# Kernel tuning notes

Hardware: AMD Instinct MI355X
Metric: run time of the kernel (lower is better)

## Reference

```python
import jax, jax.numpy as jnp
import numpy as np

B, L = 131072, 24  # batch size, number of links (= n_dofs, all revolute)


def _skew(v):
    # v: [L, 3] -> [L, 3, 3] cross-product matrices
    zeros = jnp.zeros_like(v[:, 0])
    return jnp.stack([
        jnp.stack([zeros, -v[:, 2], v[:, 1]], axis=-1),
        jnp.stack([v[:, 2], zeros, -v[:, 0]], axis=-1),
        jnp.stack([-v[:, 1], v[:, 0], zeros], axis=-1),
    ], axis=-2)


def setup_inputs() -> dict:
    key = jax.random.key(0)
    k1, k2, k3, k4 = jax.random.split(key, 4)
    q = jax.random.normal(k1, (B, L), dtype=jnp.float32)
    qd = jax.random.normal(k2, (B, L), dtype=jnp.float32)
    axes = jax.random.normal(k3, (L, 3), dtype=jnp.float32)   # joint axes (normalized in reference)
    t_fix = jax.random.normal(k4, (L, 3), dtype=jnp.float32)  # fixed parent->joint translations
    return {"q": q, "qd": qd, "axes": axes, "t_fix": t_fix}


def reference(q, qd, axes, t_fix):
    # Stateless forward kinematics for all links of a serial revolute chain.
    # joint_pose_i = Trans(t_fix_i) @ Rot(axis_i, q_i);  pose_i = pose_{i-1} @ joint_pose_i
    dtype = q.dtype
    a = axes / jnp.linalg.norm(axes, axis=-1, keepdims=True)  # [L,3]
    K = _skew(a)                                              # [L,3,3]
    KK = jnp.einsum('lij,ljk->lik', K, K)
    s = jnp.sin(q)[..., None, None]                           # [B,L,1,1]
    c = jnp.cos(q)[..., None, None]
    I3 = jnp.eye(3, dtype=dtype)
    # Rodrigues: per-joint rotation [B,L,3,3]
    R_joint = I3 + s * K[None] + (1.0 - c) * KK[None]

    def step(carry, x):
        Rp, tp = carry          # parent pose: [B,3,3], [B,3]
        Rj, tf = x              # joint rotation [B,3,3], fixed translation [3]
        tc = tp + jnp.einsum('bij,j->bi', Rp, tf)
        Rc = jnp.einsum('bij,bjk->bik', Rp, Rj)
        return (Rc, tc), (Rc, tc)

    R0 = jnp.broadcast_to(I3, (q.shape[0], 3, 3))
    t0 = jnp.zeros((q.shape[0], 3), dtype=dtype)
    Rj_seq = jnp.moveaxis(R_joint, 1, 0)                      # [L,B,3,3]
    _, (Rs, ts) = jax.lax.scan(step, (R0, t0), (Rj_seq, t_fix))
    Rs = jnp.moveaxis(Rs, 0, 1)                               # [B,L,3,3]
    ts = jnp.moveaxis(ts, 0, 1)                               # [B,L,3]
    top = jnp.concatenate([Rs, ts[..., None]], axis=-1)       # [B,L,3,4]
    bottom = jnp.broadcast_to(jnp.array([0., 0., 0., 1.], dtype=dtype),
                              top.shape[:-2] + (1, 4))
    return jnp.concatenate([top, bottom], axis=-2)            # [B,L,4,4]
```

## Files before the change

kernel.cpp:

```cpp
#include <hip/hip_runtime.h>


typedef float v4 __attribute__((ext_vector_type(4)));

constexpr int L = 24;

__global__ __launch_bounds__(256, 4) void fk_kernel(
    const float* __restrict__ q,
    const float* __restrict__ axes,
    const float* __restrict__ tfix,
    float* __restrict__ out,
    int nb)
{
    __shared__ float s_lnk[L][12];

    if (threadIdx.x < L) {
        const int l = threadIdx.x;
        float ax = axes[l * 3 + 0], ay = axes[l * 3 + 1], az = axes[l * 3 + 2];
        float inv = rsqrtf(ax * ax + ay * ay + az * az);
        ax *= inv; ay *= inv; az *= inv;
        s_lnk[l][0] = ax;             s_lnk[l][1] = ay;             s_lnk[l][2] = az;
        s_lnk[l][3] = tfix[l * 3 + 0]; s_lnk[l][4] = tfix[l * 3 + 1]; s_lnk[l][5] = tfix[l * 3 + 2];
        s_lnk[l][6] = ax * ax;        s_lnk[l][7] = ay * ay;
        s_lnk[l][8] = az * az;        s_lnk[l][9] = ax * ay;
        s_lnk[l][10] = ax * az;       s_lnk[l][11] = ay * az;
    }
    __syncthreads();

    const int tid = blockIdx.x * 256 + threadIdx.x;
    const int b = tid >> 2;
    const int r = tid & 3;
    if (b >= nb) return;

    float qv[L];
    {
        const v4* q4 = (const v4*)(q + (size_t)b * L);
        #pragma unroll
        for (int i = 0; i < L / 4; ++i) {
            v4 v = q4[i];
            qv[4 * i + 0] = v.x;
            qv[4 * i + 1] = v.y;
            qv[4 * i + 2] = v.z;
            qv[4 * i + 3] = v.w;
        }
    }

    float Ra = (r == 0) ? 1.f : 0.f;
    float Rb = (r == 1) ? 1.f : 0.f;
    float Rc = (r == 2) ? 1.f : 0.f;
    float t  = (r == 3) ? 1.f : 0.f;

    v4* orow = (v4*)out + (size_t)b * (4 * L) + r;

    #pragma unroll
    for (int l = 0; l < L; ++l) {
        const float ax = s_lnk[l][0], ay = s_lnk[l][1], az = s_lnk[l][2];
        const float fx = s_lnk[l][3], fy = s_lnk[l][4], fz = s_lnk[l][5];
        const float xx = s_lnk[l][6], yy = s_lnk[l][7], zz = s_lnk[l][8];
        const float xy = s_lnk[l][9], xz = s_lnk[l][10], yz = s_lnk[l][11];

        float s, c;
        __sincosf(qv[l], &s, &c);
        const float omc = 1.0f - c;

        const float J00 = fmaf(omc, xx, c);
        const float J11 = fmaf(omc, yy, c);
        const float J22 = fmaf(omc, zz, c);
        const float oxy = omc * xy, oxz = omc * xz, oyz = omc * yz;
        const float sx = s * ax, sy = s * ay, sz = s * az;
        const float J01 = oxy - sz, J10 = oxy + sz;
        const float J02 = oxz + sy, J20 = oxz - sy;
        const float J12 = oyz - sx, J21 = oyz + sx;

        t = fmaf(Ra, fx, fmaf(Rb, fy, fmaf(Rc, fz, t)));

        const float na  = fmaf(Ra, J00, fmaf(Rb, J10, Rc * J20));
        const float nb_ = fmaf(Ra, J01, fmaf(Rb, J11, Rc * J21));
        const float nc  = fmaf(Ra, J02, fmaf(Rb, J12, Rc * J22));
        Ra = na; Rb = nb_; Rc = nc;

        orow[l * 4] = v4{Ra, Rb, Rc, t};
    }
}

extern "C" void kernel_launch(void* const* d_in, const int* in_sizes, int n_in,
                              void* d_out, int out_size, void* d_ws, size_t ws_size,
                              hipStream_t stream) {
    const float* q    = (const float*)d_in[0];
    const float* axes = (const float*)d_in[2];
    const float* tfix = (const float*)d_in[3];
    float* out = (float*)d_out;

    const int nb = in_sizes[0] / L;
    const long long nthreads = (long long)nb * 4;
    const int grid = (int)((nthreads + 255) / 256);
    fk_kernel<<<grid, 256, 0, stream>>>(q, axes, tfix, out, nb);
}
```

Before: 214.0 us.

## Compute full pose per thread instead of one row per thread

Switches from four threads per batch element (one output row each) to one thread per batch element that carries the full 3x3 rotation and translation. This removes the fourfold redundant q loads and sincos evaluations and vectorizes the shared-memory constant reads. In exchange each thread writes 64 contiguous bytes per link with large strides between threads, which loses store coalescing. There are also fewer threads available for latency hiding, and launch bounds are relaxed to allow more registers.

```diff
diff --git a/kernel.cpp b/kernel.cpp
--- a/kernel.cpp
+++ b/kernel.cpp
@@ -5,31 +5,30 @@
 
 constexpr int L = 24;
 
-__global__ __launch_bounds__(256, 4) void fk_kernel(
+__global__ __launch_bounds__(256, 2) void fk_kernel(
     const float* __restrict__ q,
     const float* __restrict__ axes,
     const float* __restrict__ tfix,
     float* __restrict__ out,
     int nb)
 {
-    __shared__ float s_lnk[L][12];
+    __shared__ __align__(16) float s_lnk[L][16];
 
     if (threadIdx.x < L) {
         const int l = threadIdx.x;
         float ax = axes[l * 3 + 0], ay = axes[l * 3 + 1], az = axes[l * 3 + 2];
         float inv = rsqrtf(ax * ax + ay * ay + az * az);
         ax *= inv; ay *= inv; az *= inv;
-        s_lnk[l][0] = ax;             s_lnk[l][1] = ay;             s_lnk[l][2] = az;
+        s_lnk[l][0] = ax;              s_lnk[l][1] = ay;              s_lnk[l][2] = az;
         s_lnk[l][3] = tfix[l * 3 + 0]; s_lnk[l][4] = tfix[l * 3 + 1]; s_lnk[l][5] = tfix[l * 3 + 2];
-        s_lnk[l][6] = ax * ax;        s_lnk[l][7] = ay * ay;
-        s_lnk[l][8] = az * az;        s_lnk[l][9] = ax * ay;
-        s_lnk[l][10] = ax * az;       s_lnk[l][11] = ay * az;
+        s_lnk[l][6] = ax * ax;         s_lnk[l][7] = ay * ay;
+        s_lnk[l][8] = az * az;         s_lnk[l][9] = ax * ay;
+        s_lnk[l][10] = ax * az;        s_lnk[l][11] = ay * az;
+        s_lnk[l][12] = 0.f; s_lnk[l][13] = 0.f; s_lnk[l][14] = 0.f; s_lnk[l][15] = 0.f;
     }
     __syncthreads();
 
-    const int tid = blockIdx.x * 256 + threadIdx.x;
-    const int b = tid >> 2;
-    const int r = tid & 3;
+    const int b = blockIdx.x * 256 + threadIdx.x;
     if (b >= nb) return;
 
     float qv[L];
@@ -45,19 +44,21 @@
         }
     }
 
-    float Ra = (r == 0) ? 1.f : 0.f;
-    float Rb = (r == 1) ? 1.f : 0.f;
-    float Rc = (r == 2) ? 1.f : 0.f;
-    float t  = (r == 3) ? 1.f : 0.f;
+    float R00 = 1.f, R01 = 0.f, R02 = 0.f;
+    float R10 = 0.f, R11 = 1.f, R12 = 0.f;
+    float R20 = 0.f, R21 = 0.f, R22 = 1.f;
+    float tx = 0.f, ty = 0.f, tz = 0.f;
 
-    v4* orow = (v4*)out + (size_t)b * (4 * L) + r;
+    v4* obase = (v4*)out + (size_t)b * (4 * L);
 
     #pragma unroll
     for (int l = 0; l < L; ++l) {
-        const float ax = s_lnk[l][0], ay = s_lnk[l][1], az = s_lnk[l][2];
-        const float fx = s_lnk[l][3], fy = s_lnk[l][4], fz = s_lnk[l][5];
-        const float xx = s_lnk[l][6], yy = s_lnk[l][7], zz = s_lnk[l][8];
-        const float xy = s_lnk[l][9], xz = s_lnk[l][10], yz = s_lnk[l][11];
+        const v4 c0 = *(const v4*)&s_lnk[l][0];
+        const v4 c1 = *(const v4*)&s_lnk[l][4];
+        const v4 c2 = *(const v4*)&s_lnk[l][8];
+        const float ax = c0.x, ay = c0.y, az = c0.z, fx = c0.w;
+        const float fy = c1.x, fz = c1.y, xx = c1.z, yy = c1.w;
+        const float zz = c2.x, xy = c2.y, xz = c2.z, yz = c2.w;
 
         float s, c;
         __sincosf(qv[l], &s, &c);
@@ -72,14 +73,27 @@
         const float J02 = oxz + sy, J20 = oxz - sy;
         const float J12 = oyz - sx, J21 = oyz + sx;
 
-        t = fmaf(Ra, fx, fmaf(Rb, fy, fmaf(Rc, fz, t)));
+        tx = fmaf(R00, fx, fmaf(R01, fy, fmaf(R02, fz, tx)));
+        ty = fmaf(R10, fx, fmaf(R11, fy, fmaf(R12, fz, ty)));
+        tz = fmaf(R20, fx, fmaf(R21, fy, fmaf(R22, fz, tz)));
 
-        const float na  = fmaf(Ra, J00, fmaf(Rb, J10, Rc * J20));
-        const float nb_ = fmaf(Ra, J01, fmaf(Rb, J11, Rc * J21));
-        const float nc  = fmaf(Ra, J02, fmaf(Rb, J12, Rc * J22));
-        Ra = na; Rb = nb_; Rc = nc;
+        const float n00 = fmaf(R00, J00, fmaf(R01, J10, R02 * J20));
+        const float n01 = fmaf(R00, J01, fmaf(R01, J11, R02 * J21));
+        const float n02 = fmaf(R00, J02, fmaf(R01, J12, R02 * J22));
+        const float n10 = fmaf(R10, J00, fmaf(R11, J10, R12 * J20));
+        const float n11 = fmaf(R10, J01, fmaf(R11, J11, R12 * J21));
+        const float n12 = fmaf(R10, J02, fmaf(R11, J12, R12 * J22));
+        const float n20 = fmaf(R20, J00, fmaf(R21, J10, R22 * J20));
+        const float n21 = fmaf(R20, J01, fmaf(R21, J11, R22 * J21));
+        const float n22 = fmaf(R20, J02, fmaf(R21, J12, R22 * J22));
+        R00 = n00; R01 = n01; R02 = n02;
+        R10 = n10; R11 = n11; R12 = n12;
+        R20 = n20; R21 = n21; R22 = n22;
 
-        orow[l * 4] = v4{Ra, Rb, Rc, t};
+        obase[l * 4 + 0] = v4{R00, R01, R02, tx};
+        obase[l * 4 + 1] = v4{R10, R11, R12, ty};
+        obase[l * 4 + 2] = v4{R20, R21, R22, tz};
+        obase[l * 4 + 3] = v4{0.f, 0.f, 0.f, 1.f};
     }
 }
 
@@ -92,7 +106,6 @@
     float* out = (float*)d_out;
 
     const int nb = in_sizes[0] / L;
-    const long long nthreads = (long long)nb * 4;
-    const int grid = (int)((nthreads + 255) / 256);
+    const int grid = (nb + 255) / 256;
     fk_kernel<<<grid, 256, 0, stream>>>(q, axes, tfix, out, nb);
 }
```

Result: slower. 251.6 us (+17.6%).

## Stage output poses through LDS per wave for coalesced nontemporal stores

Applied to the files above, without the earlier changes.

Each wave writes its computed 4x4 poses for 16 batch elements into a padded LDS buffer in chunks of 8 links. It then reads them back so consecutive lanes write contiguous 16-byte segments of global memory with nontemporal stores. The goal is to replace the previous strided per-thread row stores with fully coalesced writes. The q load is also moved ahead of the shared-memory setup barrier, and link constants are read as vector LDS loads. The cost is extra LDS traffic and footprint, and the wave-level sync relies only on a compiler memory barrier within the wave.

```diff
diff --git a/kernel.cpp b/kernel.cpp
--- a/kernel.cpp
+++ b/kernel.cpp
@@ -4,6 +4,11 @@
 typedef float v4 __attribute__((ext_vector_type(4)));
 
 constexpr int L = 24;
+constexpr int CHUNK = 8;
+constexpr int NCHUNK = L / CHUNK;
+constexpr int CW  = CHUNK * 16;
+constexpr int CWP = CW + 4;
+constexpr int WAVE_WORDS = 16 * CWP;
 
 __global__ __launch_bounds__(256, 4) void fk_kernel(
     const float* __restrict__ q,
@@ -12,74 +17,110 @@
     float* __restrict__ out,
     int nb)
 {
-    __shared__ float s_lnk[L][12];
+    __shared__ __align__(16) float s_lnk[L][16];
+    __shared__ __align__(16) float s_buf[4 * WAVE_WORDS];
 
-    if (threadIdx.x < L) {
-        const int l = threadIdx.x;
-        float ax = axes[l * 3 + 0], ay = axes[l * 3 + 1], az = axes[l * 3 + 2];
-        float inv = rsqrtf(ax * ax + ay * ay + az * az);
-        ax *= inv; ay *= inv; az *= inv;
-        s_lnk[l][0] = ax;             s_lnk[l][1] = ay;             s_lnk[l][2] = az;
-        s_lnk[l][3] = tfix[l * 3 + 0]; s_lnk[l][4] = tfix[l * 3 + 1]; s_lnk[l][5] = tfix[l * 3 + 2];
-        s_lnk[l][6] = ax * ax;        s_lnk[l][7] = ay * ay;
-        s_lnk[l][8] = az * az;        s_lnk[l][9] = ax * ay;
-        s_lnk[l][10] = ax * az;       s_lnk[l][11] = ay * az;
-    }
-    __syncthreads();
-
-    const int tid = blockIdx.x * 256 + threadIdx.x;
-    const int b = tid >> 2;
-    const int r = tid & 3;
-    if (b >= nb) return;
+    const int tid  = threadIdx.x;
+    const int wave = tid >> 6;
+    const int lane = tid & 63;
+    const int e    = lane >> 2;
+    const int r    = lane & 3;
+    const int wave_elem0 = blockIdx.x * 64 + wave * 16;
+    const int b = wave_elem0 + e;
 
     float qv[L];
-    {
+    if (b < nb) {
         const v4* q4 = (const v4*)(q + (size_t)b * L);
         #pragma unroll
         for (int i = 0; i < L / 4; ++i) {
             v4 v = q4[i];
-            qv[4 * i + 0] = v.x;
-            qv[4 * i + 1] = v.y;
-            qv[4 * i + 2] = v.z;
-            qv[4 * i + 3] = v.w;
+            qv[4*i+0] = v.x; qv[4*i+1] = v.y; qv[4*i+2] = v.z; qv[4*i+3] = v.w;
         }
     }
+
+    if (tid < L) {
+        const int l = tid;
+        float ax = axes[l*3+0], ay = axes[l*3+1], az = axes[l*3+2];
+        float inv = rsqrtf(ax*ax + ay*ay + az*az);
+        ax *= inv; ay *= inv; az *= inv;
+        s_lnk[l][0] = ax;            s_lnk[l][1] = ay;            s_lnk[l][2] = az;
+        s_lnk[l][3] = tfix[l*3+0];   s_lnk[l][4] = tfix[l*3+1];   s_lnk[l][5] = tfix[l*3+2];
+        s_lnk[l][6] = ax*ax;         s_lnk[l][7] = ay*ay;
+        s_lnk[l][8] = az*az;         s_lnk[l][9] = ax*ay;
+        s_lnk[l][10] = ax*az;        s_lnk[l][11] = ay*az;
+        s_lnk[l][12] = 0.f; s_lnk[l][13] = 0.f; s_lnk[l][14] = 0.f; s_lnk[l][15] = 0.f;
+    }
+    __syncthreads();
 
     float Ra = (r == 0) ? 1.f : 0.f;
     float Rb = (r == 1) ? 1.f : 0.f;
     float Rc = (r == 2) ? 1.f : 0.f;
     float t  = (r == 3) ? 1.f : 0.f;
 
-    v4* orow = (v4*)out + (size_t)b * (4 * L) + r;
+    float* wbuf = s_buf + wave * WAVE_WORDS;
+    v4* lrow = (v4*)(wbuf + e * CWP + r * 4);
 
     #pragma unroll
-    for (int l = 0; l < L; ++l) {
-        const float ax = s_lnk[l][0], ay = s_lnk[l][1], az = s_lnk[l][2];
-        const float fx = s_lnk[l][3], fy = s_lnk[l][4], fz = s_lnk[l][5];
-        const float xx = s_lnk[l][6], yy = s_lnk[l][7], zz = s_lnk[l][8];
-        const float xy = s_lnk[l][9], xz = s_lnk[l][10], yz = s_lnk[l][11];
+    for (int chunk = 0; chunk < NCHUNK; ++chunk) {
+        if (b < nb) {
+            #pragma unroll
+            for (int lc = 0; lc < CHUNK; ++lc) {
+                const int l = chunk * CHUNK + lc;
+                const v4 c0 = *(const v4*)&s_lnk[l][0];
+                const v4 c1 = *(const v4*)&s_lnk[l][4];
+                const v4 c2 = *(const v4*)&s_lnk[l][8];
+                const float ax = c0.x, ay = c0.y, az = c0.z, fx = c0.w;
+                const float fy = c1.x, fz = c1.y, xx = c1.z, yy = c1.w;
+                const float zz = c2.x, xy = c2.y, xz = c2.z, yz = c2.w;
 
-        float s, c;
-        __sincosf(qv[l], &s, &c);
-        const float omc = 1.0f - c;
+                float s, c;
+                __sincosf(qv[l], &s, &c);
+                const float omc = 1.0f - c;
 
-        const float J00 = fmaf(omc, xx, c);
-        const float J11 = fmaf(omc, yy, c);
-        const float J22 = fmaf(omc, zz, c);
-        const float oxy = omc * xy, oxz = omc * xz, oyz = omc * yz;
-        const float sx = s * ax, sy = s * ay, sz = s * az;
-        const float J01 = oxy - sz, J10 = oxy + sz;
-        const float J02 = oxz + sy, J20 = oxz - sy;
-        const float J12 = oyz - sx, J21 = oyz + sx;
+                const float J00 = fmaf(omc, xx, c);
+                const float J11 = fmaf(omc, yy, c);
+                const float J22 = fmaf(omc, zz, c);
+                const float oxy = omc * xy, oxz = omc * xz, oyz = omc * yz;
+                const float sx = s * ax, sy = s * ay, sz = s * az;
+                const float J01 = oxy - sz, J10 = oxy + sz;
+                const float J02 = oxz + sy, J20 = oxz - sy;
+                const float J12 = oyz - sx, J21 = oyz + sx;
 
-        t = fmaf(Ra, fx, fmaf(Rb, fy, fmaf(Rc, fz, t)));
+                t = fmaf(Ra, fx, fmaf(Rb, fy, fmaf(Rc, fz, t)));
 
-        const float na  = fmaf(Ra, J00, fmaf(Rb, J10, Rc * J20));
-        const float nb_ = fmaf(Ra, J01, fmaf(Rb, J11, Rc * J21));
-        const float nc  = fmaf(Ra, J02, fmaf(Rb, J12, Rc * J22));
-        Ra = na; Rb = nb_; Rc = nc;
+                const float na  = fmaf(Ra, J00, fmaf(Rb, J10, Rc * J20));
+                const float nb_ = fmaf(Ra, J01, fmaf(Rb, J11, Rc * J21));
+                const float nc  = fmaf(Ra, J02, fmaf(Rb, J12, Rc * J22));
+                Ra = na; Rb = nb_; Rc = nc;
 
-        orow[l * 4] = v4{Ra, Rb, Rc, t};
+                lrow[lc * 4] = v4{Ra, Rb, Rc, t};
+            }
+        }
+
+        asm volatile("" ::: "memory");
+
+        float* gbase = out + (size_t)wave_elem0 * 384 + chunk * CW;
+        if (wave_elem0 + 15 < nb) {
+            #pragma unroll
+            for (int j = 0; j < CHUNK; ++j) {
+                const unsigned w = j * 256 + lane * 4;
+                const unsigned elem = w >> 7;
+                const unsigned rem  = w & 127u;
+                v4 v = *(const v4*)(wbuf + elem * CWP + rem);
+                __builtin_nontemporal_store(v, (v4*)(gbase + (size_t)elem * 384 + rem));
+            }
+        } else if (wave_elem0 < nb) {
+            #pragma unroll
+            for (int j = 0; j < CHUNK; ++j) {
+                const unsigned w = j * 256 + lane * 4;
+                const unsigned elem = w >> 7;
+                const unsigned rem  = w & 127u;
+                if (wave_elem0 + (int)elem < nb) {
+                    v4 v = *(const v4*)(wbuf + elem * CWP + rem);
+                    __builtin_nontemporal_store(v, (v4*)(gbase + (size_t)elem * 384 + rem));
+                }
+            }
+        }
     }
 }
 
@@ -92,7 +133,6 @@
     float* out = (float*)d_out;
 
     const int nb = in_sizes[0] / L;
-    const long long nthreads = (long long)nb * 4;
-    const int grid = (int)((nthreads + 255) / 256);
+    const int grid = (nb + 63) / 64;
     fk_kernel<<<grid, 256, 0, stream>>>(q, axes, tfix, out, nb);
 }
```

Result: slower. 224.0 us (+4.7%).

## Use persistent grid-stride blocks with prefetch of next batch's joint angles

Applied to the files above, without the earlier changes.

Launches a fixed grid of 512 blocks that loop over batch elements with a grid stride instead of one thread group per element. Each iteration prefetches the next element's joint angles into registers so the global load overlaps the current chain computation. Per-link constants are padded to 16 floats so they can be read from shared memory as vector loads. The risk is fewer resident waves to hide the latency of the output stores, which dominate this bandwidth-bound kernel, plus extra register pressure from the prefetch buffers.

```diff
diff --git a/kernel.cpp b/kernel.cpp
--- a/kernel.cpp
+++ b/kernel.cpp
@@ -4,6 +4,8 @@
 typedef float v4 __attribute__((ext_vector_type(4)));
 
 constexpr int L = 24;
+constexpr int BLOCKS = 512;
+constexpr int NGROUPS = BLOCKS * 64;
 
 __global__ __launch_bounds__(256, 4) void fk_kernel(
     const float* __restrict__ q,
@@ -12,74 +14,97 @@
     float* __restrict__ out,
     int nb)
 {
-    __shared__ float s_lnk[L][12];
+    __shared__ __align__(16) float s_lnk[L][16];
 
     if (threadIdx.x < L) {
         const int l = threadIdx.x;
-        float ax = axes[l * 3 + 0], ay = axes[l * 3 + 1], az = axes[l * 3 + 2];
-        float inv = rsqrtf(ax * ax + ay * ay + az * az);
+        float ax = axes[l*3+0], ay = axes[l*3+1], az = axes[l*3+2];
+        float inv = rsqrtf(ax*ax + ay*ay + az*az);
         ax *= inv; ay *= inv; az *= inv;
-        s_lnk[l][0] = ax;             s_lnk[l][1] = ay;             s_lnk[l][2] = az;
-        s_lnk[l][3] = tfix[l * 3 + 0]; s_lnk[l][4] = tfix[l * 3 + 1]; s_lnk[l][5] = tfix[l * 3 + 2];
-        s_lnk[l][6] = ax * ax;        s_lnk[l][7] = ay * ay;
-        s_lnk[l][8] = az * az;        s_lnk[l][9] = ax * ay;
-        s_lnk[l][10] = ax * az;       s_lnk[l][11] = ay * az;
+        s_lnk[l][0] = ax;            s_lnk[l][1] = ay;            s_lnk[l][2] = az;
+        s_lnk[l][3] = tfix[l*3+0];   s_lnk[l][4] = tfix[l*3+1];   s_lnk[l][5] = tfix[l*3+2];
+        s_lnk[l][6] = ax*ax;         s_lnk[l][7] = ay*ay;
+        s_lnk[l][8] = az*az;         s_lnk[l][9] = ax*ay;
+        s_lnk[l][10] = ax*az;        s_lnk[l][11] = ay*az;
+        s_lnk[l][12] = 0.f; s_lnk[l][13] = 0.f; s_lnk[l][14] = 0.f; s_lnk[l][15] = 0.f;
     }
     __syncthreads();
 
     const int tid = blockIdx.x * 256 + threadIdx.x;
-    const int b = tid >> 2;
-    const int r = tid & 3;
+    const int gid = tid >> 2;
+    const int r   = tid & 3;
+
+    int b = gid;
     if (b >= nb) return;
 
-    float qv[L];
-    {
-        const v4* q4 = (const v4*)(q + (size_t)b * L);
+    const v4* q4 = (const v4*)q;
+
+    v4 nq0 = q4[(size_t)b * 6 + 0];
+    v4 nq1 = q4[(size_t)b * 6 + 1];
+    v4 nq2 = q4[(size_t)b * 6 + 2];
+    v4 nq3 = q4[(size_t)b * 6 + 3];
+    v4 nq4 = q4[(size_t)b * 6 + 4];
+    v4 nq5 = q4[(size_t)b * 6 + 5];
+
+    while (b < nb) {
+        float qv[L];
+        qv[0]=nq0.x; qv[1]=nq0.y; qv[2]=nq0.z; qv[3]=nq0.w;
+        qv[4]=nq1.x; qv[5]=nq1.y; qv[6]=nq1.z; qv[7]=nq1.w;
+        qv[8]=nq2.x; qv[9]=nq2.y; qv[10]=nq2.z; qv[11]=nq2.w;
+        qv[12]=nq3.x; qv[13]=nq3.y; qv[14]=nq3.z; qv[15]=nq3.w;
+        qv[16]=nq4.x; qv[17]=nq4.y; qv[18]=nq4.z; qv[19]=nq4.w;
+        qv[20]=nq5.x; qv[21]=nq5.y; qv[22]=nq5.z; qv[23]=nq5.w;
+
+        const int bn = b + NGROUPS;
+        if (bn < nb) {
+            nq0 = q4[(size_t)bn * 6 + 0];
+            nq1 = q4[(size_t)bn * 6 + 1];
+            nq2 = q4[(size_t)bn * 6 + 2];
+            nq3 = q4[(size_t)bn * 6 + 3];
+            nq4 = q4[(size_t)bn * 6 + 4];
+            nq5 = q4[(size_t)bn * 6 + 5];
+        }
+
+        float Ra = (r == 0) ? 1.f : 0.f;
+        float Rb = (r == 1) ? 1.f : 0.f;
+        float Rc = (r == 2) ? 1.f : 0.f;
+        float t  = (r == 3) ? 1.f : 0.f;
+
+        v4* orow = (v4*)out + (size_t)b * (4 * L) + r;
+
         #pragma unroll
-        for (int i = 0; i < L / 4; ++i) {
-            v4 v = q4[i];
-            qv[4 * i + 0] = v.x;
-            qv[4 * i + 1] = v.y;
-            qv[4 * i + 2] = v.z;
-            qv[4 * i + 3] = v.w;
+        for (int l = 0; l < L; ++l) {
+            const v4 c0 = *(const v4*)&s_lnk[l][0];
+            const v4 c1 = *(const v4*)&s_lnk[l][4];
+            const v4 c2 = *(const v4*)&s_lnk[l][8];
+            const float ax = c0.x, ay = c0.y, az = c0.z, fx = c0.w;
+            const float fy = c1.x, fz = c1.y, xx = c1.z, yy = c1.w;
+            const float zz = c2.x, xy = c2.y, xz = c2.z, yz = c2.w;
+
+            float s, c;
+            __sincosf(qv[l], &s, &c);
+            const float omc = 1.0f - c;
+
+            const float J00 = fmaf(omc, xx, c);
+            const float J11 = fmaf(omc, yy, c);
+            const float J22 = fmaf(omc, zz, c);
+            const float oxy = omc * xy, oxz = omc * xz, oyz = omc * yz;
+            const float sx = s * ax, sy = s * ay, sz = s * az;
+            const float J01 = oxy - sz, J10 = oxy + sz;
+            const float J02 = oxz + sy, J20 = oxz - sy;
+            const float J12 = oyz - sx, J21 = oyz + sx;
+
+            t = fmaf(Ra, fx, fmaf(Rb, fy, fmaf(Rc, fz, t)));
+
+            const float na  = fmaf(Ra, J00, fmaf(Rb, J10, Rc * J20));
+            const float nb_ = fmaf(Ra, J01, fmaf(Rb, J11, Rc * J21));
+            const float nc  = fmaf(Ra, J02, fmaf(Rb, J12, Rc * J22));
+            Ra = na; Rb = nb_; Rc = nc;
+
+            orow[l * 4] = v4{Ra, Rb, Rc, t};
         }
-    }
 
-    float Ra = (r == 0) ? 1.f : 0.f;
-    float Rb = (r == 1) ? 1.f : 0.f;
-    float Rc = (r == 2) ? 1.f : 0.f;
-    float t  = (r == 3) ? 1.f : 0.f;
-
-    v4* orow = (v4*)out + (size_t)b * (4 * L) + r;
-
-    #pragma unroll
-    for (int l = 0; l < L; ++l) {
-        const float ax = s_lnk[l][0], ay = s_lnk[l][1], az = s_lnk[l][2];
-        const float fx = s_lnk[l][3], fy = s_lnk[l][4], fz = s_lnk[l][5];
-        const float xx = s_lnk[l][6], yy = s_lnk[l][7], zz = s_lnk[l][8];
-        const float xy = s_lnk[l][9], xz = s_lnk[l][10], yz = s_lnk[l][11];
-
-        float s, c;
-        __sincosf(qv[l], &s, &c);
-        const float omc = 1.0f - c;
-
-        const float J00 = fmaf(omc, xx, c);
-        const float J11 = fmaf(omc, yy, c);
-        const float J22 = fmaf(omc, zz, c);
-        const float oxy = omc * xy, oxz = omc * xz, oyz = omc * yz;
-        const float sx = s * ax, sy = s * ay, sz = s * az;
-        const float J01 = oxy - sz, J10 = oxy + sz;
-        const float J02 = oxz + sy, J20 = oxz - sy;
-        const float J12 = oyz - sx, J21 = oyz + sx;
-
-        t = fmaf(Ra, fx, fmaf(Rb, fy, fmaf(Rc, fz, t)));
-
-        const float na  = fmaf(Ra, J00, fmaf(Rb, J10, Rc * J20));
-        const float nb_ = fmaf(Ra, J01, fmaf(Rb, J11, Rc * J21));
-        const float nc  = fmaf(Ra, J02, fmaf(Rb, J12, Rc * J22));
-        Ra = na; Rb = nb_; Rc = nc;
-
-        orow[l * 4] = v4{Ra, Rb, Rc, t};
+        b = bn;
     }
 }
 
@@ -92,7 +117,5 @@
     float* out = (float*)d_out;
 
     const int nb = in_sizes[0] / L;
-    const long long nthreads = (long long)nb * 4;
-    const int grid = (int)((nthreads + 255) / 256);
-    fk_kernel<<<grid, 256, 0, stream>>>(q, axes, tfix, out, nb);
+    fk_kernel<<<BLOCKS, 256, 0, stream>>>(q, axes, tfix, out, nb);
 }
```

New measurement: 512.3 us. +139.4%, slower.
